# Performance work log

Hardware: AMD Instinct MI355X
Metric: run time of the kernel (lower is better)

The kernel has to match this reference:

```python
import jax, jax.numpy as jnp
import numpy as np

B, T, I, S, H = 32, 8192, 256, 256, 256
NEG = 1e30


def setup_inputs() -> dict:
    key = jax.random.key(0)
    ks = jax.random.split(key, 8)
    x = jax.random.normal(ks[0], (B, T, I), dtype=jnp.float32)
    init = jax.random.normal(ks[1], (B, S), dtype=jnp.float32)
    mask = (jax.random.uniform(ks[2], (B, T)) > 0.1).astype(jnp.float32)
    W1 = jax.random.normal(ks[3], (H, S + I), dtype=jnp.float32) * (1.0 / np.sqrt(S + I))
    W2 = jax.random.normal(ks[4], (1, H), dtype=jnp.float32) * (1.0 / np.sqrt(H))
    w_ih = jax.random.normal(ks[5], (3 * S, I), dtype=jnp.float32) * (1.0 / np.sqrt(I))
    w_hh = jax.random.normal(ks[6], (3 * S, S), dtype=jnp.float32) * (1.0 / np.sqrt(S))
    b_ih = jnp.zeros((3 * S,), dtype=jnp.float32)
    b_hh = jnp.zeros((3 * S,), dtype=jnp.float32)
    return {"x": x, "init": init, "mask": mask, "W1": W1, "W2": W2,
            "w_ih": w_ih, "w_hh": w_hh, "b_ih": b_ih, "b_hh": b_hh}


def _pointer(x, state, mask, W1, W2):
    # concat([state_expanded, input], dim=2) @ W1.T == state @ W1[:, :S].T + x @ W1[:, S:].T
    Ws, Wi = W1[:, :S], W1[:, S:]
    h = jnp.tanh(jnp.einsum('bti,hi->bth', x, Wi) + (state @ Ws.T)[:, None, :])  # [B,T,H]
    att = jnp.einsum('bth,oh->bto', h, W2)[..., 0]  # [B,T]
    logit = att - NEG * (1.0 - mask)
    p = jax.nn.softmax(logit, axis=1)
    out = jnp.einsum('bt,bti->bi', p, x)
    return out, logit


def _gru_cell(inp, h, w_ih, w_hh, b_ih, b_hh):
    gi = inp @ w_ih.T + b_ih  # [B, 3S]
    gh = h @ w_hh.T + b_hh
    i_r, i_z, i_n = jnp.split(gi, 3, axis=1)
    h_r, h_z, h_n = jnp.split(gh, 3, axis=1)
    r = jax.nn.sigmoid(i_r + h_r)
    z = jax.nn.sigmoid(i_z + h_z)
    n = jnp.tanh(i_n + r * h_n)
    return (1.0 - z) * n + z * h


def reference(x, init, mask, W1, W2, w_ih, w_hh, b_ih, b_hh):
    # eval mode: all dropout masks are identity (dropout=0.0)
    out, logit1 = _pointer(x, init, mask, W1, W2)
    state = _gru_cell(out, init, w_ih, w_hh, b_ih, b_hh)
    _, logit2 = _pointer(x, state, mask, W1, W2)
    return (logit1, logit2)
```

## Files before the change

kernel.cpp:

```cpp
#include <hip/hip_runtime.h>
#include <hip/hip_bf16.h>
#include <stdint.h>

#define BB 32
#define TT 8192
#define II 256
#define SS 256
#define HH 256
#define NEGC 1e30f

typedef __bf16 bf16x8 __attribute__((ext_vector_type(8)));
typedef __bf16 bf16x4 __attribute__((ext_vector_type(4)));
typedef float f32x4 __attribute__((ext_vector_type(4)));

__device__ __forceinline__ float fast_tanh(float x) {
    float e = __expf(2.f * x);
    return 1.f - 2.f * __builtin_amdgcn_rcpf(e + 1.f);
}
__device__ __forceinline__ float fast_sigmoid(float x) {
    return __builtin_amdgcn_rcpf(1.f + __expf(-x));
}

__global__ __launch_bounds__(256) void prep_kernel(const float* __restrict__ W1,
                                                   const float* __restrict__ init,
                                                   __bf16* __restrict__ wi,
                                                   float* __restrict__ sws) {
    __shared__ float sv[32 * 257];
    int tid = threadIdx.x;
    if (blockIdx.x < 256) {
        int idx = blockIdx.x * 256 + tid;
        int h = idx >> 8, k = idx & 255;
        wi[idx] = (__bf16)W1[h * 512 + 256 + k];
        return;
    }
    for (int e = tid; e < 8192; e += 256) {
        int b = e >> 8, s = e & 255;
        sv[b * 257 + s] = init[b * 256 + s];
    }
    __syncthreads();
    int hl = tid >> 4, bg = tid & 15;
    int h = (blockIdx.x - 256) * 16 + hl;
    const float* w1r = W1 + (size_t)h * 512;
    float a0 = 0.f, a1 = 0.f;
#pragma unroll 4
    for (int s = 0; s < 256; ++s) {
        float w = w1r[s];
        a0 += w * sv[(bg * 2 + 0) * 257 + s];
        a1 += w * sv[(bg * 2 + 1) * 257 + s];
    }
    sws[(bg * 2 + 0) * 256 + h] = a0;
    sws[(bg * 2 + 1) * 256 + h] = a1;
}

__global__ __launch_bounds__(256) void sws_slice_kernel(const float* __restrict__ state,
                                                        const float* __restrict__ W1,
                                                        float* __restrict__ sws) {
    __shared__ float sv[32 * 257];
    int tid = threadIdx.x;
    for (int e = tid; e < 8192; e += 256) {
        int b = e >> 8, s = e & 255;
        sv[b * 257 + s] = state[b * 256 + s];
    }
    __syncthreads();
    int hl = tid >> 4, bg = tid & 15;
    int h = blockIdx.x * 16 + hl;
    const float* w1r = W1 + (size_t)h * 512;
    float a0 = 0.f, a1 = 0.f;
#pragma unroll 4
    for (int s = 0; s < 256; ++s) {
        float w = w1r[s];
        a0 += w * sv[(bg * 2 + 0) * 257 + s];
        a1 += w * sv[(bg * 2 + 1) * 257 + s];
    }
    sws[(bg * 2 + 0) * 256 + h] = a0;
    sws[(bg * 2 + 1) * 256 + h] = a1;
}

template <int MODE>
__global__ __launch_bounds__(256, 3) void att_kernel(
    const float* __restrict__ x, const __bf16* __restrict__ xbf_in,
    __bf16* __restrict__ xbf_out, const __bf16* __restrict__ wi,
    const float* __restrict__ w2, const float* __restrict__ sws,
    const float* __restrict__ mask, float* __restrict__ logit_out) {
    __shared__ char xs[64 * 512];
    __shared__ float attp[4][64];

    const int tid = threadIdx.x;
    const int lane = tid & 63, w = tid >> 6;
    const size_t rowbase = (size_t)blockIdx.x * 64;
    const int b = (int)(rowbase >> 13);

    if (MODE == 1) {
        const char* src = (const char*)xbf_in + rowbase * 512;
#pragma unroll
        for (int it = 0; it < 8; ++it) {
            int L = (it * 256 + tid) * 16;
            bf16x8 v = *(const bf16x8*)(src + L);
            int row = L >> 9, kb = L & 511;
            *(bf16x8*)(xs + row * 512 + (kb ^ ((row & 7) << 4))) = v;
        }
    } else {
        const float* src = x + rowbase * 256;
#pragma unroll
        for (int it = 0; it < 8; ++it) {
            int L = (it * 256 + tid) * 16;
            int e = L >> 1;
            float4 f0 = *(const float4*)(src + e);
            float4 f1 = *(const float4*)(src + e + 4);
            bf16x8 v;
            v[0] = (__bf16)f0.x; v[1] = (__bf16)f0.y; v[2] = (__bf16)f0.z; v[3] = (__bf16)f0.w;
            v[4] = (__bf16)f1.x; v[5] = (__bf16)f1.y; v[6] = (__bf16)f1.z; v[7] = (__bf16)f1.w;
            int row = L >> 9, kb = L & 511;
            *(bf16x8*)(xs + row * 512 + (kb ^ ((row & 7) << 4))) = v;
            if (MODE == 0)
                *(bf16x8*)((char*)xbf_out + rowbase * 512 + L) = v;
        }
    }

    const int l15 = lane & 15, lg = lane >> 4;
    float w2v[4], swsv[4];
#pragma unroll
    for (int fn = 0; fn < 4; ++fn) {
        int h = w * 64 + fn * 16 + l15;
        w2v[fn] = w2[h];
        swsv[fn] = sws[b * 256 + h];
    }

    __syncthreads();

    f32x4 acc[4][4] = {};
    const char* wib = (const char*)wi + (size_t)(w * 64 + l15) * 512 + lg * 16;
    bf16x8 bnext[4];
#pragma unroll
    for (int fn = 0; fn < 4; ++fn)
        bnext[fn] = *(const bf16x8*)(wib + fn * 8192);
#pragma unroll
    for (int kk = 0; kk < 8; ++kk) {
        bf16x8 bcur[4];
#pragma unroll
        for (int fn = 0; fn < 4; ++fn) bcur[fn] = bnext[fn];
        if (kk < 7) {
#pragma unroll
            for (int fn = 0; fn < 4; ++fn)
                bnext[fn] = *(const bf16x8*)(wib + fn * 8192 + (kk + 1) * 64);
        }
        bf16x8 afrag[4];
#pragma unroll
        for (int fm = 0; fm < 4; ++fm) {
            int row = fm * 16 + l15;
            int kb = kk * 64 + lg * 16;
            afrag[fm] = *(const bf16x8*)(xs + row * 512 + (kb ^ ((row & 7) << 4)));
        }
#pragma unroll
        for (int fm = 0; fm < 4; ++fm)
#pragma unroll
            for (int fn = 0; fn < 4; ++fn)
                acc[fm][fn] = __builtin_amdgcn_mfma_f32_16x16x32_bf16(
                    afrag[fm], bcur[fn], acc[fm][fn], 0, 0, 0);
    }

    const bool hi8 = (l15 & 8) != 0, hi4 = (l15 & 4) != 0;
    const int ridx = ((l15 & 8) >> 2) | ((l15 & 4) >> 2);
#pragma unroll
    for (int fm = 0; fm < 4; ++fm) {
        float part[4];
#pragma unroll
        for (int r = 0; r < 4; ++r) {
            float s = 0.f;
#pragma unroll
            for (int fn = 0; fn < 4; ++fn) {
                float hv = acc[fm][fn][r] + swsv[fn];
                s += w2v[fn] * fast_tanh(hv);
            }
            part[r] = s;
        }
        float s0 = hi8 ? part[0] : part[2];
        float s1 = hi8 ? part[1] : part[3];
        float r0 = __shfl_xor(s0, 8, 64);
        float r1 = __shfl_xor(s1, 8, 64);
        float a0 = (hi8 ? part[2] : part[0]) + r0;
        float a1 = (hi8 ? part[3] : part[1]) + r1;
        float s2 = hi4 ? a0 : a1;
        float r2 = __shfl_xor(s2, 4, 64);
        float bsum = (hi4 ? a1 : a0) + r2;
        bsum += __shfl_xor(bsum, 2, 64);
        bsum += __shfl_xor(bsum, 1, 64);
        if ((l15 & 3) == 0) attp[w][fm * 16 + lg * 4 + ridx] = bsum;
    }
    __syncthreads();
    if (tid < 64) {
        float att = attp[0][tid] + attp[1][tid] + attp[2][tid] + attp[3][tid];
        float mv = mask[rowbase + tid];
        logit_out[rowbase + tid] = att - NEGC * (1.f - mv);
    }
}

__global__ __launch_bounds__(256) void chunkstat_kernel(const float* __restrict__ logit,
                                                        float2* __restrict__ stat) {
    __shared__ float redm[4], reds[4];
    int bc = blockIdx.x, tid = threadIdx.x;
    const float* lp = logit + (size_t)bc * 1024;
    float4 v = *(const float4*)(lp + tid * 4);
    float m = fmaxf(fmaxf(v.x, v.y), fmaxf(v.z, v.w));
#pragma unroll
    for (int o = 1; o < 64; o <<= 1) m = fmaxf(m, __shfl_xor(m, o, 64));
    if ((tid & 63) == 0) redm[tid >> 6] = m;
    __syncthreads();
    m = fmaxf(fmaxf(redm[0], redm[1]), fmaxf(redm[2], redm[3]));
    float s = __expf(v.x - m) + __expf(v.y - m) + __expf(v.z - m) + __expf(v.w - m);
#pragma unroll
    for (int o = 1; o < 64; o <<= 1) s += __shfl_xor(s, o, 64);
    if ((tid & 63) == 0) reds[tid >> 6] = s;
    __syncthreads();
    if (tid == 0) {
        float2 st;
        st.x = m;
        st.y = reds[0] + reds[1] + reds[2] + reds[3];
        stat[bc] = st;
    }
}

template <int MODE>
__global__ __launch_bounds__(256) void outpart_kernel(
    const float* __restrict__ logit, const float2* __restrict__ stat,
    const float* __restrict__ xf, const __bf16* __restrict__ xbf,
    float* __restrict__ out_part) {
    int b = blockIdx.x >> 5, c = blockIdx.x & 31;
    int tid = threadIdx.x;
    int ig = tid & 31, tg = tid >> 5;
    __shared__ float pl[256];
    __shared__ float sacc[8][264];
    float m = -3.4e38f;
#pragma unroll
    for (int cc = 0; cc < 8; ++cc) m = fmaxf(m, stat[b * 8 + cc].x);
    float ssum = 0.f;
#pragma unroll
    for (int cc = 0; cc < 8; ++cc) {
        float2 st = stat[b * 8 + cc];
        ssum += st.y * __expf(st.x - m);
    }
    float invs = 1.f / ssum;
    const size_t tbase = (size_t)b * TT + (size_t)c * 256;
    pl[tid] = __expf(logit[tbase + tid] - m) * invs;
    __syncthreads();
    float a[8] = {};
    if (MODE == 0) {
        const __bf16* xp = xbf + tbase * 256 + ig * 8;
        for (int t = tg; t < 256; t += 8) {
            float pv = pl[t];
            bf16x8 v = *(const bf16x8*)(xp + (size_t)t * 256);
#pragma unroll
            for (int j = 0; j < 8; ++j) a[j] += pv * (float)v[j];
        }
    } else {
        const float* xp = xf + tbase * 256 + ig * 8;
        for (int t = tg; t < 256; t += 8) {
            float pv = pl[t];
            float4 f0 = *(const float4*)(xp + (size_t)t * 256);
            float4 f1 = *(const float4*)(xp + (size_t)t * 256 + 4);
            a[0] += pv * f0.x; a[1] += pv * f0.y; a[2] += pv * f0.z; a[3] += pv * f0.w;
            a[4] += pv * f1.x; a[5] += pv * f1.y; a[6] += pv * f1.z; a[7] += pv * f1.w;
        }
    }
#pragma unroll
    for (int j = 0; j < 8; ++j) sacc[tg][ig * 8 + j] = a[j];
    __syncthreads();
    float s = 0.f;
#pragma unroll
    for (int j = 0; j < 8; ++j) s += sacc[j][tid];
    out_part[(size_t)(b * 32 + c) * 256 + tid] = s;
}

__global__ __launch_bounds__(256) void outsum_kernel(const float* __restrict__ out_part,
                                                     float* __restrict__ out_sum) {
    int b = blockIdx.x, i = threadIdx.x;
    float s = 0.f;
#pragma unroll
    for (int c = 0; c < 32; ++c) s += out_part[(size_t)(b * 32 + c) * 256 + i];
    out_sum[b * 256 + i] = s;
}

__global__ __launch_bounds__(256) void gru_gemm_kernel(
    const float* __restrict__ out_sum, const float* __restrict__ init,
    const float* __restrict__ w_ih, const float* __restrict__ w_hh,
    const float* __restrict__ b_ih, const float* __restrict__ b_hh,
    float* __restrict__ gi, float* __restrict__ gh) {
    __shared__ float outv[32 * 257];
    __shared__ float initv[32 * 257];
    int tid = threadIdx.x;
    for (int e = tid; e < 8192; e += 256) {
        int b = e >> 8, i = e & 255;
        outv[b * 257 + i] = out_sum[b * 256 + i];
        initv[b * 257 + i] = init[b * 256 + i];
    }
    __syncthreads();
    int kl = tid >> 4, bg = tid & 15;
    int k = blockIdx.x * 16 + kl;
    const float* wir = w_ih + (size_t)k * 256;
    const float* whr = w_hh + (size_t)k * 256;
    float gia0 = b_ih[k], gia1 = gia0;
    float gha0 = b_hh[k], gha1 = gha0;
#pragma unroll 4
    for (int i = 0; i < 256; ++i) {
        float wiv = wir[i], whv = whr[i];
        gia0 += wiv * outv[(bg * 2 + 0) * 257 + i];
        gia1 += wiv * outv[(bg * 2 + 1) * 257 + i];
        gha0 += whv * initv[(bg * 2 + 0) * 257 + i];
        gha1 += whv * initv[(bg * 2 + 1) * 257 + i];
    }
    gi[k * 32 + bg * 2 + 0] = gia0;
    gi[k * 32 + bg * 2 + 1] = gia1;
    gh[k * 32 + bg * 2 + 0] = gha0;
    gh[k * 32 + bg * 2 + 1] = gha1;
}

__global__ __launch_bounds__(256) void gru_point_kernel(
    const float* __restrict__ gi, const float* __restrict__ gh,
    const float* __restrict__ init, float* __restrict__ state) {
    int b = blockIdx.x, s = threadIdx.x;
    float gir = gi[s * 32 + b], giz = gi[(256 + s) * 32 + b], gin = gi[(512 + s) * 32 + b];
    float ghr = gh[s * 32 + b], ghz = gh[(256 + s) * 32 + b], ghn = gh[(512 + s) * 32 + b];
    float r = fast_sigmoid(gir + ghr);
    float z = fast_sigmoid(giz + ghz);
    float n = fast_tanh(gin + r * ghn);
    float h0 = init[b * 256 + s];
    state[b * 256 + s] = (1.f - z) * n + z * h0;
}

extern "C" void kernel_launch(void* const* d_in, const int* in_sizes, int n_in,
                              void* d_out, int out_size, void* d_ws, size_t ws_size,
                              hipStream_t stream) {
    const float* x = (const float*)d_in[0];
    const float* init = (const float*)d_in[1];
    const float* mask = (const float*)d_in[2];
    const float* W1 = (const float*)d_in[3];
    const float* W2 = (const float*)d_in[4];
    const float* w_ih = (const float*)d_in[5];
    const float* w_hh = (const float*)d_in[6];
    const float* b_ih = (const float*)d_in[7];
    const float* b_hh = (const float*)d_in[8];
    float* out = (float*)d_out;

    char* ws = (char*)d_ws;
    size_t off = 0;
    auto alloc = [&](size_t sz) {
        char* p = ws + off;
        off += (sz + 255) & ~(size_t)255;
        return p;
    };
    __bf16* wi = (__bf16*)alloc((size_t)HH * II * 2);
    float* sws1 = (float*)alloc(BB * 256 * 4);
    float* sws2 = (float*)alloc(BB * 256 * 4);
    float* out_part = (float*)alloc((size_t)BB * 32 * 256 * 4);
    float* out_sum = (float*)alloc(BB * 256 * 4);
    float2* stat = (float2*)alloc(BB * 8 * 8);
    float* gi_buf = (float*)alloc(768 * 32 * 4);
    float* gh_buf = (float*)alloc(768 * 32 * 4);
    float* state_buf = (float*)alloc(BB * 256 * 4);
    __bf16* xbf = (__bf16*)alloc((size_t)BB * TT * II * 2);
    const bool big = (off <= ws_size);
    (void)in_sizes; (void)n_in; (void)out_size;

    prep_kernel<<<272, 256, 0, stream>>>(W1, init, wi, sws1);

    const int ntiles = BB * TT / 64;
    if (big)
        att_kernel<0><<<ntiles, 256, 0, stream>>>(x, nullptr, xbf, wi, W2, sws1, mask, out);
    else
        att_kernel<2><<<ntiles, 256, 0, stream>>>(x, nullptr, nullptr, wi, W2, sws1, mask, out);

    chunkstat_kernel<<<256, 256, 0, stream>>>(out, stat);

    if (big)
        outpart_kernel<0><<<1024, 256, 0, stream>>>(out, stat, nullptr, xbf, out_part);
    else
        outpart_kernel<2><<<1024, 256, 0, stream>>>(out, stat, x, nullptr, out_part);

    outsum_kernel<<<32, 256, 0, stream>>>(out_part, out_sum);
    gru_gemm_kernel<<<48, 256, 0, stream>>>(out_sum, init, w_ih, w_hh, b_ih, b_hh,
                                            gi_buf, gh_buf);
    gru_point_kernel<<<32, 256, 0, stream>>>(gi_buf, gh_buf, init, state_buf);
    sws_slice_kernel<<<16, 256, 0, stream>>>(state_buf, W1, sws2);

    if (big)
        att_kernel<1><<<ntiles, 256, 0, stream>>>(nullptr, xbf, nullptr, wi, W2, sws2, mask,
                                                  out + (size_t)BB * TT);
    else
        att_kernel<2><<<ntiles, 256, 0, stream>>>(x, nullptr, nullptr, wi, W2, sws2, mask,
                                                  out + (size_t)BB * TT);
}
```

Before: 565.0 us.

## Cache x·Wi product for second pass, store x as fp8, fuse softmax stats

The first attention pass now writes the bf16 x·Wi GEMM result to workspace, so the second pass only applies the new state bias, tanh and W2 reduction instead of redoing the GEMM. The bf16 copy of x used by the weighted sum is replaced with an fp8 copy, halving that traffic. Per-tile max and sum-exp statistics are computed inside the first attention kernel, removing the separate chunkstat kernel. The outpart kernel is regridded to combine the finer-grained statistics. The fp8 storage of x and the bf16 rounding of the cached pre-activations add precision risk to the pooled vector and to the second logits.

```diff
diff --git a/kernel.cpp b/kernel.cpp
--- a/kernel.cpp
+++ b/kernel.cpp
@@ -12,6 +12,7 @@
 typedef __bf16 bf16x8 __attribute__((ext_vector_type(8)));
 typedef __bf16 bf16x4 __attribute__((ext_vector_type(4)));
 typedef float f32x4 __attribute__((ext_vector_type(4)));
+typedef float f32x2 __attribute__((ext_vector_type(2)));
 
 __device__ __forceinline__ float fast_tanh(float x) {
     float e = __expf(2.f * x);
@@ -77,11 +78,12 @@
 }
 
 template <int MODE>
-__global__ __launch_bounds__(256, 3) void att_kernel(
-    const float* __restrict__ x, const __bf16* __restrict__ xbf_in,
-    __bf16* __restrict__ xbf_out, const __bf16* __restrict__ wi,
+__global__ __launch_bounds__(256, 3) void att1_kernel(
+    const float* __restrict__ x, const __bf16* __restrict__ wi,
     const float* __restrict__ w2, const float* __restrict__ sws,
-    const float* __restrict__ mask, float* __restrict__ logit_out) {
+    const float* __restrict__ mask, float* __restrict__ logit_out,
+    __bf16* __restrict__ xwi, unsigned char* __restrict__ xfp8,
+    float2* __restrict__ tstat) {
     __shared__ char xs[64 * 512];
     __shared__ float attp[4][64];
 
@@ -90,16 +92,7 @@
     const size_t rowbase = (size_t)blockIdx.x * 64;
     const int b = (int)(rowbase >> 13);
 
-    if (MODE == 1) {
-        const char* src = (const char*)xbf_in + rowbase * 512;
-#pragma unroll
-        for (int it = 0; it < 8; ++it) {
-            int L = (it * 256 + tid) * 16;
-            bf16x8 v = *(const bf16x8*)(src + L);
-            int row = L >> 9, kb = L & 511;
-            *(bf16x8*)(xs + row * 512 + (kb ^ ((row & 7) << 4))) = v;
-        }
-    } else {
+    {
         const float* src = x + rowbase * 256;
 #pragma unroll
         for (int it = 0; it < 8; ++it) {
@@ -112,8 +105,14 @@
             v[4] = (__bf16)f1.x; v[5] = (__bf16)f1.y; v[6] = (__bf16)f1.z; v[7] = (__bf16)f1.w;
             int row = L >> 9, kb = L & 511;
             *(bf16x8*)(xs + row * 512 + (kb ^ ((row & 7) << 4))) = v;
-            if (MODE == 0)
-                *(bf16x8*)((char*)xbf_out + rowbase * 512 + L) = v;
+            if (MODE == 0) {
+                unsigned int lo = __builtin_amdgcn_cvt_pk_fp8_f32(f0.x, f0.y, 0u, false);
+                lo = __builtin_amdgcn_cvt_pk_fp8_f32(f0.z, f0.w, lo, true);
+                unsigned int hi = __builtin_amdgcn_cvt_pk_fp8_f32(f1.x, f1.y, 0u, false);
+                hi = __builtin_amdgcn_cvt_pk_fp8_f32(f1.z, f1.w, hi, true);
+                uint2 pk; pk.x = lo; pk.y = hi;
+                *(uint2*)(xfp8 + rowbase * 256 + e) = pk;
+            }
         }
     }
 
@@ -157,6 +156,23 @@
             for (int fn = 0; fn < 4; ++fn)
                 acc[fm][fn] = __builtin_amdgcn_mfma_f32_16x16x32_bf16(
                     afrag[fm], bcur[fn], acc[fm][fn], 0, 0, 0);
+    }
+
+    if (MODE == 0) {
+#pragma unroll
+        for (int fm = 0; fm < 4; ++fm) {
+            bf16x8 p0, p1;
+#pragma unroll
+            for (int r = 0; r < 4; ++r) {
+                p0[0 * 4 + r] = (__bf16)acc[fm][0][r];
+                p0[1 * 4 + r] = (__bf16)acc[fm][1][r];
+                p1[0 * 4 + r] = (__bf16)acc[fm][2][r];
+                p1[1 * 4 + r] = (__bf16)acc[fm][3][r];
+            }
+            size_t base = (((size_t)blockIdx.x * 16 + w * 4 + fm) * 128 + lane * 2) * 8;
+            *(bf16x8*)(xwi + base) = p0;
+            *(bf16x8*)(xwi + base + 8) = p1;
+        }
     }
 
     const bool hi8 = (l15 & 8) != 0, hi4 = (l15 & 4) != 0;
@@ -191,70 +207,117 @@
     if (tid < 64) {
         float att = attp[0][tid] + attp[1][tid] + attp[2][tid] + attp[3][tid];
         float mv = mask[rowbase + tid];
+        float lgt = att - NEGC * (1.f - mv);
+        logit_out[rowbase + tid] = lgt;
+        float m = lgt;
+#pragma unroll
+        for (int o = 1; o < 64; o <<= 1) m = fmaxf(m, __shfl_xor(m, o, 64));
+        float e = __expf(lgt - m);
+#pragma unroll
+        for (int o = 1; o < 64; o <<= 1) e += __shfl_xor(e, o, 64);
+        if (tid == 0) {
+            float2 st; st.x = m; st.y = e;
+            tstat[blockIdx.x] = st;
+        }
+    }
+}
+
+__global__ __launch_bounds__(256) void att2_kernel(
+    const __bf16* __restrict__ xwi, const float* __restrict__ w2,
+    const float* __restrict__ sws, const float* __restrict__ mask,
+    float* __restrict__ logit_out) {
+    __shared__ float attp[4][64];
+    const int tid = threadIdx.x;
+    const int lane = tid & 63, w = tid >> 6;
+    const size_t rowbase = (size_t)blockIdx.x * 64;
+    const int b = (int)(rowbase >> 13);
+    const int l15 = lane & 15, lg = lane >> 4;
+    float w2v[4], swsv[4];
+#pragma unroll
+    for (int fn = 0; fn < 4; ++fn) {
+        int h = w * 64 + fn * 16 + l15;
+        w2v[fn] = w2[h];
+        swsv[fn] = sws[b * 256 + h];
+    }
+    const bool hi8 = (l15 & 8) != 0, hi4 = (l15 & 4) != 0;
+    const int ridx = ((l15 & 8) >> 2) | ((l15 & 4) >> 2);
+#pragma unroll
+    for (int fm = 0; fm < 4; ++fm) {
+        size_t base = (((size_t)blockIdx.x * 16 + w * 4 + fm) * 128 + lane * 2) * 8;
+        bf16x8 p0 = *(const bf16x8*)(xwi + base);
+        bf16x8 p1 = *(const bf16x8*)(xwi + base + 8);
+        float part[4];
+#pragma unroll
+        for (int r = 0; r < 4; ++r) {
+            float s = 0.f;
+            s += w2v[0] * fast_tanh((float)p0[0 * 4 + r] + swsv[0]);
+            s += w2v[1] * fast_tanh((float)p0[1 * 4 + r] + swsv[1]);
+            s += w2v[2] * fast_tanh((float)p1[0 * 4 + r] + swsv[2]);
+            s += w2v[3] * fast_tanh((float)p1[1 * 4 + r] + swsv[3]);
+            part[r] = s;
+        }
+        float s0 = hi8 ? part[0] : part[2];
+        float s1 = hi8 ? part[1] : part[3];
+        float r0 = __shfl_xor(s0, 8, 64);
+        float r1 = __shfl_xor(s1, 8, 64);
+        float a0 = (hi8 ? part[2] : part[0]) + r0;
+        float a1 = (hi8 ? part[3] : part[1]) + r1;
+        float s2 = hi4 ? a0 : a1;
+        float r2 = __shfl_xor(s2, 4, 64);
+        float bsum = (hi4 ? a1 : a0) + r2;
+        bsum += __shfl_xor(bsum, 2, 64);
+        bsum += __shfl_xor(bsum, 1, 64);
+        if ((l15 & 3) == 0) attp[w][fm * 16 + lg * 4 + ridx] = bsum;
+    }
+    __syncthreads();
+    if (tid < 64) {
+        float att = attp[0][tid] + attp[1][tid] + attp[2][tid] + attp[3][tid];
+        float mv = mask[rowbase + tid];
         logit_out[rowbase + tid] = att - NEGC * (1.f - mv);
-    }
-}
-
-__global__ __launch_bounds__(256) void chunkstat_kernel(const float* __restrict__ logit,
-                                                        float2* __restrict__ stat) {
-    __shared__ float redm[4], reds[4];
-    int bc = blockIdx.x, tid = threadIdx.x;
-    const float* lp = logit + (size_t)bc * 1024;
-    float4 v = *(const float4*)(lp + tid * 4);
-    float m = fmaxf(fmaxf(v.x, v.y), fmaxf(v.z, v.w));
-#pragma unroll
-    for (int o = 1; o < 64; o <<= 1) m = fmaxf(m, __shfl_xor(m, o, 64));
-    if ((tid & 63) == 0) redm[tid >> 6] = m;
-    __syncthreads();
-    m = fmaxf(fmaxf(redm[0], redm[1]), fmaxf(redm[2], redm[3]));
-    float s = __expf(v.x - m) + __expf(v.y - m) + __expf(v.z - m) + __expf(v.w - m);
-#pragma unroll
-    for (int o = 1; o < 64; o <<= 1) s += __shfl_xor(s, o, 64);
-    if ((tid & 63) == 0) reds[tid >> 6] = s;
-    __syncthreads();
-    if (tid == 0) {
-        float2 st;
-        st.x = m;
-        st.y = reds[0] + reds[1] + reds[2] + reds[3];
-        stat[bc] = st;
     }
 }
 
 template <int MODE>
 __global__ __launch_bounds__(256) void outpart_kernel(
-    const float* __restrict__ logit, const float2* __restrict__ stat,
-    const float* __restrict__ xf, const __bf16* __restrict__ xbf,
+    const float* __restrict__ logit, const float2* __restrict__ tstat,
+    const float* __restrict__ xf, const unsigned char* __restrict__ xfp8,
     float* __restrict__ out_part) {
-    int b = blockIdx.x >> 5, c = blockIdx.x & 31;
+    int b = blockIdx.x >> 6, c = blockIdx.x & 63;
     int tid = threadIdx.x;
     int ig = tid & 31, tg = tid >> 5;
-    __shared__ float pl[256];
+    __shared__ float pl[128];
     __shared__ float sacc[8][264];
-    float m = -3.4e38f;
-#pragma unroll
-    for (int cc = 0; cc < 8; ++cc) m = fmaxf(m, stat[b * 8 + cc].x);
-    float ssum = 0.f;
-#pragma unroll
-    for (int cc = 0; cc < 8; ++cc) {
-        float2 st = stat[b * 8 + cc];
-        ssum += st.y * __expf(st.x - m);
-    }
-    float invs = 1.f / ssum;
-    const size_t tbase = (size_t)b * TT + (size_t)c * 256;
-    pl[tid] = __expf(logit[tbase + tid] - m) * invs;
+    float M = -3.4e38f;
+#pragma unroll 8
+    for (int i = 0; i < 128; ++i) M = fmaxf(M, tstat[b * 128 + i].x);
+    float S = 0.f;
+#pragma unroll 8
+    for (int i = 0; i < 128; ++i) {
+        float2 st = tstat[b * 128 + i];
+        S += st.y * __expf(st.x - M);
+    }
+    float invs = 1.f / S;
+    const size_t tbase = (size_t)b * TT + (size_t)c * 128;
+    if (tid < 128) pl[tid] = __expf(logit[tbase + tid] - M) * invs;
     __syncthreads();
     float a[8] = {};
     if (MODE == 0) {
-        const __bf16* xp = xbf + tbase * 256 + ig * 8;
-        for (int t = tg; t < 256; t += 8) {
+        const unsigned char* xp = xfp8 + tbase * 256 + ig * 8;
+        for (int t = tg; t < 128; t += 8) {
             float pv = pl[t];
-            bf16x8 v = *(const bf16x8*)(xp + (size_t)t * 256);
-#pragma unroll
-            for (int j = 0; j < 8; ++j) a[j] += pv * (float)v[j];
+            uint2 v = *(const uint2*)(xp + (size_t)t * 256);
+            f32x2 d0 = __builtin_amdgcn_cvt_pk_f32_fp8(v.x, false);
+            f32x2 d1 = __builtin_amdgcn_cvt_pk_f32_fp8(v.x, true);
+            f32x2 d2 = __builtin_amdgcn_cvt_pk_f32_fp8(v.y, false);
+            f32x2 d3 = __builtin_amdgcn_cvt_pk_f32_fp8(v.y, true);
+            a[0] += pv * d0[0]; a[1] += pv * d0[1];
+            a[2] += pv * d1[0]; a[3] += pv * d1[1];
+            a[4] += pv * d2[0]; a[5] += pv * d2[1];
+            a[6] += pv * d3[0]; a[7] += pv * d3[1];
         }
     } else {
         const float* xp = xf + tbase * 256 + ig * 8;
-        for (int t = tg; t < 256; t += 8) {
+        for (int t = tg; t < 128; t += 8) {
             float pv = pl[t];
             float4 f0 = *(const float4*)(xp + (size_t)t * 256);
             float4 f1 = *(const float4*)(xp + (size_t)t * 256 + 4);
@@ -268,7 +331,7 @@
     float s = 0.f;
 #pragma unroll
     for (int j = 0; j < 8; ++j) s += sacc[j][tid];
-    out_part[(size_t)(b * 32 + c) * 256 + tid] = s;
+    out_part[(size_t)(b * 64 + c) * 256 + tid] = s;
 }
 
 __global__ __launch_bounds__(256) void outsum_kernel(const float* __restrict__ out_part,
@@ -276,7 +339,7 @@
     int b = blockIdx.x, i = threadIdx.x;
     float s = 0.f;
 #pragma unroll
-    for (int c = 0; c < 32; ++c) s += out_part[(size_t)(b * 32 + c) * 256 + i];
+    for (int c = 0; c < 64; ++c) s += out_part[(size_t)(b * 64 + c) * 256 + i];
     out_sum[b * 256 + i] = s;
 }
 
@@ -351,13 +414,14 @@
     __bf16* wi = (__bf16*)alloc((size_t)HH * II * 2);
     float* sws1 = (float*)alloc(BB * 256 * 4);
     float* sws2 = (float*)alloc(BB * 256 * 4);
-    float* out_part = (float*)alloc((size_t)BB * 32 * 256 * 4);
+    float* out_part = (float*)alloc((size_t)BB * 64 * 256 * 4);
     float* out_sum = (float*)alloc(BB * 256 * 4);
-    float2* stat = (float2*)alloc(BB * 8 * 8);
+    float2* tstat = (float2*)alloc(4096 * 8);
     float* gi_buf = (float*)alloc(768 * 32 * 4);
     float* gh_buf = (float*)alloc(768 * 32 * 4);
     float* state_buf = (float*)alloc(BB * 256 * 4);
-    __bf16* xbf = (__bf16*)alloc((size_t)BB * TT * II * 2);
+    __bf16* xwi = (__bf16*)alloc((size_t)BB * TT * HH * 2);
+    unsigned char* xfp8 = (unsigned char*)alloc((size_t)BB * TT * II);
     const bool big = (off <= ws_size);
     (void)in_sizes; (void)n_in; (void)out_size;
 
@@ -365,16 +429,16 @@
 
     const int ntiles = BB * TT / 64;
     if (big)
-        att_kernel<0><<<ntiles, 256, 0, stream>>>(x, nullptr, xbf, wi, W2, sws1, mask, out);
+        att1_kernel<0><<<ntiles, 256, 0, stream>>>(x, wi, W2, sws1, mask, out,
+                                                   xwi, xfp8, tstat);
     else
-        att_kernel<2><<<ntiles, 256, 0, stream>>>(x, nullptr, nullptr, wi, W2, sws1, mask, out);
-
-    chunkstat_kernel<<<256, 256, 0, stream>>>(out, stat);
+        att1_kernel<2><<<ntiles, 256, 0, stream>>>(x, wi, W2, sws1, mask, out,
+                                                   nullptr, nullptr, tstat);
 
     if (big)
-        outpart_kernel<0><<<1024, 256, 0, stream>>>(out, stat, nullptr, xbf, out_part);
+        outpart_kernel<0><<<2048, 256, 0, stream>>>(out, tstat, nullptr, xfp8, out_part);
     else
-        outpart_kernel<2><<<1024, 256, 0, stream>>>(out, stat, x, nullptr, out_part);
+        outpart_kernel<2><<<2048, 256, 0, stream>>>(out, tstat, x, nullptr, out_part);
 
     outsum_kernel<<<32, 256, 0, stream>>>(out_part, out_sum);
     gru_gemm_kernel<<<48, 256, 0, stream>>>(out_sum, init, w_ih, w_hh, b_ih, b_hh,
@@ -383,9 +447,10 @@
     sws_slice_kernel<<<16, 256, 0, stream>>>(state_buf, W1, sws2);
 
     if (big)
-        att_kernel<1><<<ntiles, 256, 0, stream>>>(nullptr, xbf, nullptr, wi, W2, sws2, mask,
-                                                  out + (size_t)BB * TT);
+        att2_kernel<<<ntiles, 256, 0, stream>>>(xwi, W2, sws2, mask,
+                                                out + (size_t)BB * TT);
     else
-        att_kernel<2><<<ntiles, 256, 0, stream>>>(x, nullptr, nullptr, wi, W2, sws2, mask,
-                                                  out + (size_t)BB * TT);
-}
+        att1_kernel<2><<<ntiles, 256, 0, stream>>>(x, wi, W2, sws2, mask,
+                                                   out + (size_t)BB * TT,
+                                                   nullptr, nullptr, tstat);
+}
```

New measurement: 557.1 us. Within noise of the previous version (-1.4%).
